# Optimization experiments

Measured on AMD Instinct MI355X. Metric: run time of the kernel, lower is better.

The kernel has to match this reference:

```python
import jax, jax.numpy as jnp
import numpy as np

B_SZ, SEQ, H, P = 4, 8192, 512, 256


def _s5(x, lam_re, lam_im, log_dt, b_re, b_im, c_re, c_im, d):
    """Single-direction S5 diagonal SSM. x: [B,L,H] -> y: [B,L,H]."""
    lam = lam_re + 1j * lam_im                      # [P] complex diagonal A
    dt = jnp.exp(log_dt)                            # [P] ZOH timestep
    a_bar = jnp.exp(lam * dt)                       # [P] discretized A
    b_bar = ((a_bar - 1.0) / lam)[:, None] * (b_re + 1j * b_im)  # [P,H]
    bu = jnp.einsum('blh,ph->blp', x.astype(b_bar.dtype), b_bar)  # [B,L,P]
    a_el = jnp.broadcast_to(a_bar, bu.shape)        # time-invariant A per step

    def comb(e1, e2):  # associative combine for linear recurrence
        a1, s1 = e1
        a2, s2 = e2
        return (a1 * a2, a2 * s1 + s2)

    _, states = jax.lax.associative_scan(comb, (a_el, bu), axis=1)  # [B,L,P]
    c = c_re + 1j * c_im                            # [H,P]
    return jnp.einsum('blp,hp->blh', states, c).real + x * d


def setup_inputs() -> dict:
    key = jax.random.key(0)
    ks = jax.random.split(key, 10)
    return {
        'x': jax.random.normal(ks[0], (B_SZ, SEQ, H), dtype=jnp.float32),
        'Lambda_re': -0.1 - 0.5 * jax.random.uniform(ks[1], (2, P), dtype=jnp.float32),
        'Lambda_im': jnp.pi * jax.random.normal(ks[2], (2, P), dtype=jnp.float32),
        'log_dt': jnp.log(0.001) + (jnp.log(0.1) - jnp.log(0.001)) * jax.random.uniform(ks[3], (2, P), dtype=jnp.float32),
        'B_re': jax.random.normal(ks[4], (2, P, H), dtype=jnp.float32) / np.sqrt(H),
        'B_im': jax.random.normal(ks[5], (2, P, H), dtype=jnp.float32) / np.sqrt(H),
        'C_re': jax.random.normal(ks[6], (2, H, P), dtype=jnp.float32) / np.sqrt(P),
        'C_im': jax.random.normal(ks[7], (2, H, P), dtype=jnp.float32) / np.sqrt(P),
        'D': jax.random.normal(ks[8], (2, H), dtype=jnp.float32),
    }


def reference(x, Lambda_re, Lambda_im, log_dt, B_re, B_im, C_re, C_im, D):
    # fwd(x) + flip(bwd(flip(x)))
    y_f = _s5(x, Lambda_re[0], Lambda_im[0], log_dt[0], B_re[0], B_im[0], C_re[0], C_im[0], D[0])
    x_r = x[:, ::-1]
    y_b = _s5(x_r, Lambda_re[1], Lambda_im[1], log_dt[1], B_re[1], B_im[1], C_re[1], C_im[1], D[1])[:, ::-1]
    return y_f + y_b
```

## Files before the change

kernel.cpp:

```cpp
#include <hip/hip_runtime.h>
#include <math.h>

typedef unsigned short ushort_t;
typedef __bf16 bf16x8 __attribute__((ext_vector_type(8)));
typedef ushort_t ushort8v __attribute__((ext_vector_type(8)));
typedef float f32x4 __attribute__((ext_vector_type(4)));

#define B_SZ   4
#define SEQ    8192
#define M_ROWS (B_SZ * SEQ)
#define CH     128
#define NC     (SEQ / CH)

__device__ __forceinline__ ushort_t f2bf(float f) {
    unsigned u = __float_as_uint(f);
    u = u + 0x7fffu + ((u >> 16) & 1u);
    return (ushort_t)(u >> 16);
}
__device__ __forceinline__ float bf2f(ushort_t b) {
    return __uint_as_float(((unsigned)b) << 16);
}

__device__ __forceinline__ void load16_lds(const void* g, void* l) {
    __builtin_amdgcn_global_load_lds(
        (const __attribute__((address_space(1))) unsigned int*)g,
        (__attribute__((address_space(3))) unsigned int*)l, 16, 0, 0);
}

__global__ void prep_kernel(const float* __restrict__ Lre,
                            const float* __restrict__ Lim,
                            const float* __restrict__ ldt,
                            const float* __restrict__ Bre,
                            const float* __restrict__ Bim,
                            const float* __restrict__ Cre,
                            const float* __restrict__ Cim,
                            float* __restrict__ abar,
                            float* __restrict__ apow,
                            ushort_t* __restrict__ Bmat,
                            ushort_t* __restrict__ Cmat) {
    int idx = blockIdx.x * 256 + threadIdx.x;
    int h = idx & 511;
    int p = (idx >> 9) & 255;
    int d = idx >> 17;
    int ip = d * 256 + p;
    float lr = Lre[ip], li = Lim[ip];
    float dt = expf(ldt[ip]);
    float e   = expf(lr * dt);
    float ang = li * dt;
    float ar = e * cosf(ang), ai = e * sinf(ang);
    float nr = ar - 1.0f, ni = ai;
    float den = lr * lr + li * li;
    float cr = (nr * lr + ni * li) / den;
    float ci = (ni * lr - nr * li) / den;
    float br = Bre[idx], bi = Bim[idx];
    Bmat[(d * 512 + 2 * p) * 512 + h]     = f2bf(cr * br - ci * bi);
    Bmat[(d * 512 + 2 * p + 1) * 512 + h] = f2bf(cr * bi + ci * br);
    if (h == 0) {
        int o = d * 512 + 2 * p;
        abar[o] = ar;  abar[o + 1] = ai;
        float eC = expf(lr * dt * (float)CH);
        float aC = ang * (float)CH;
        apow[o] = eC * cosf(aC);  apow[o + 1] = eC * sinf(aC);
    }
    int p2 = idx & 255;
    int h2 = (idx >> 8) & 511;
    int d2 = idx >> 17;
    Cmat[h2 * 1024 + d2 * 512 + 2 * p2]     = f2bf(Cre[idx]);
    Cmat[h2 * 1024 + d2 * 512 + 2 * p2 + 1] = f2bf(-Cim[idx]);
}

__global__ void conv_x_kernel(const float* __restrict__ x,
                              ushort_t* __restrict__ X16) {
    int i = blockIdx.x * 256 + threadIdx.x;
    float4 v = ((const float4*)x)[i];
    ushort_t o[4] = {f2bf(v.x), f2bf(v.y), f2bf(v.z), f2bf(v.w)};
    *(uint2*)&X16[(size_t)i * 4] = *(const uint2*)o;
}

template<int EPI, int KD_, int NT>
__global__ __launch_bounds__(256)
void gemm_mfma(const ushort_t* __restrict__ A, const ushort_t* __restrict__ Bm,
               ushort_t* __restrict__ Cb, float* __restrict__ Cf,
               const float* __restrict__ X, const float* __restrict__ Dv) {
    __shared__ ushort_t As[128 * 32];
    __shared__ ushort_t Bs[128 * 32];
    const int tid  = threadIdx.x;
    const int lane = tid & 63;
    const int wv   = tid >> 6;
    const int wrow = wv >> 1, wcol = wv & 1;
    const int l15  = lane & 15, lq = lane >> 4;

    const int lin = blockIdx.x;
    const int xcd = lin & 7;
    const int j   = lin >> 3;
    const int mt  = xcd * 32 + j / NT;
    const int nt  = j % NT;
    const int m0 = mt * 128;
    const int n0 = nt * 128;
    const int CN = NT * 128;

    f32x4 acc[4][4];
#pragma unroll
    for (int i = 0; i < 4; ++i)
#pragma unroll
        for (int jj = 0; jj < 4; ++jj)
            acc[i][jj] = (f32x4){0.f, 0.f, 0.f, 0.f};

    const int grow_l = lane >> 2;
    const int gk8    = (lane & 3) * 8;

    const ushort_t* aF = As + (wrow * 64 + l15) * 32 + lq * 8;
    const ushort_t* bF = Bs + (wcol * 64 + l15) * 32 + lq * 8;

    for (int kt = 0; kt < KD_; kt += 32) {
        __syncthreads();
#pragma unroll
        for (int j2 = 0; j2 < 2; ++j2) {
            const int r0 = j2 * 64 + wv * 16;
            load16_lds(&A[(size_t)(m0 + r0 + grow_l) * KD_ + kt + gk8],
                       (void*)&As[r0 * 32]);
            load16_lds(&Bm[(size_t)(n0 + r0 + grow_l) * KD_ + kt + gk8],
                       (void*)&Bs[r0 * 32]);
        }
        __syncthreads();

        bf16x8 af[4], bfr[4];
#pragma unroll
        for (int mi = 0; mi < 4; ++mi) {
            union { ushort8v u; bf16x8 b; } cv;
            cv.u = *(const ushort8v*)(aF + mi * 512);
            af[mi] = cv.b;
        }
#pragma unroll
        for (int ni = 0; ni < 4; ++ni) {
            union { ushort8v u; bf16x8 b; } cv;
            cv.u = *(const ushort8v*)(bF + ni * 512);
            bfr[ni] = cv.b;
        }
#pragma unroll
        for (int mi = 0; mi < 4; ++mi)
#pragma unroll
            for (int ni = 0; ni < 4; ++ni)
                acc[mi][ni] = __builtin_amdgcn_mfma_f32_16x16x32_bf16(
                    af[mi], bfr[ni], acc[mi][ni], 0, 0, 0);
    }

#pragma unroll
    for (int mi = 0; mi < 4; ++mi) {
#pragma unroll
        for (int ni = 0; ni < 4; ++ni) {
            const int col = n0 + wcol * 64 + ni * 16 + l15;
            float dsum = 0.f;
            if (EPI == 1) dsum = Dv[col] + Dv[512 + col];
#pragma unroll
            for (int r = 0; r < 4; ++r) {
                const int row = m0 + wrow * 64 + mi * 16 + lq * 4 + r;
                if (EPI == 0) {
                    Cb[(size_t)row * CN + col] = f2bf(acc[mi][ni][r]);
                } else {
                    const size_t idx = (size_t)row * 512 + col;
                    Cf[idx] = acc[mi][ni][r] + X[idx] * dsum;
                }
            }
        }
    }
}

__global__ __launch_bounds__(512)
void scan_carry(const ushort_t* __restrict__ S, const float* __restrict__ abar,
                float* __restrict__ carry) {
    int b = blockIdx.x, c = blockIdx.y, t = threadIdx.x;
    int dir = t >> 8, p = t & 255;
    float ar = abar[dir * 512 + 2 * p], ai = abar[dir * 512 + 2 * p + 1];
    float sr = 0.f, si = 0.f;
    const ushort_t* base = S + ((size_t)b * SEQ + (size_t)c * CH) * 1024
                             + dir * 512 + 2 * p;
    for (int ii = 0; ii < CH; ++ii) {
        int i = dir ? (CH - 1 - ii) : ii;
        unsigned u = *(const unsigned*)(base + (size_t)i * 1024);
        float re = bf2f((ushort_t)(u & 0xffffu));
        float im = bf2f((ushort_t)(u >> 16));
        float nr = fmaf(ar, sr, fmaf(-ai, si, re));
        float ni = fmaf(ar, si, fmaf(ai, sr, im));
        sr = nr; si = ni;
    }
    int o = (b * NC + c) * 1024 + dir * 512 + 2 * p;
    carry[o] = sr; carry[o + 1] = si;
}

__global__ __launch_bounds__(512)
void scan_comb(const float* __restrict__ carry, float* __restrict__ init,
               const float* __restrict__ apow) {
    int b = blockIdx.x, t = threadIdx.x;
    int dir = t >> 8, p = t & 255;
    float pr = apow[dir * 512 + 2 * p], pi = apow[dir * 512 + 2 * p + 1];
    float sr = 0.f, si = 0.f;
    for (int cc = 0; cc < NC; ++cc) {
        int c = dir ? (NC - 1 - cc) : cc;
        int o = (b * NC + c) * 1024 + dir * 512 + 2 * p;
        init[o] = sr; init[o + 1] = si;
        float cr = carry[o], ci = carry[o + 1];
        float nr = fmaf(pr, sr, fmaf(-pi, si, cr));
        float ni = fmaf(pr, si, fmaf(pi, sr, ci));
        sr = nr; si = ni;
    }
}

__global__ __launch_bounds__(512)
void scan_final(ushort_t* __restrict__ S, const float* __restrict__ abar,
                const float* __restrict__ init) {
    int b = blockIdx.x, c = blockIdx.y, t = threadIdx.x;
    int dir = t >> 8, p = t & 255;
    float ar = abar[dir * 512 + 2 * p], ai = abar[dir * 512 + 2 * p + 1];
    int o = (b * NC + c) * 1024 + dir * 512 + 2 * p;
    float sr = init[o], si = init[o + 1];
    ushort_t* base = S + ((size_t)b * SEQ + (size_t)c * CH) * 1024
                       + dir * 512 + 2 * p;
    for (int ii = 0; ii < CH; ++ii) {
        int i = dir ? (CH - 1 - ii) : ii;
        unsigned* addr = (unsigned*)(base + (size_t)i * 1024);
        unsigned u = *addr;
        float re = bf2f((ushort_t)(u & 0xffffu));
        float im = bf2f((ushort_t)(u >> 16));
        float nr = fmaf(ar, sr, fmaf(-ai, si, re));
        float ni = fmaf(ar, si, fmaf(ai, sr, im));
        sr = nr; si = ni;
        *addr = ((unsigned)f2bf(si) << 16) | (unsigned)f2bf(sr);
    }
}

extern "C" void kernel_launch(void* const* d_in, const int* in_sizes, int n_in,
                              void* d_out, int out_size, void* d_ws, size_t ws_size,
                              hipStream_t stream) {
    const float* x   = (const float*)d_in[0];
    const float* Lre = (const float*)d_in[1];
    const float* Lim = (const float*)d_in[2];
    const float* ldt = (const float*)d_in[3];
    const float* Bre = (const float*)d_in[4];
    const float* Bim = (const float*)d_in[5];
    const float* Cre = (const float*)d_in[6];
    const float* Cim = (const float*)d_in[7];
    const float* Dv  = (const float*)d_in[8];
    float* y = (float*)d_out;
    char* ws = (char*)d_ws;

    ushort_t* SB16 = (ushort_t*)(ws);
    ushort_t* X16  = (ushort_t*)(ws + 67108864);
    ushort_t* Bm16 = (ushort_t*)(ws + 100663296);
    ushort_t* Cm16 = (ushort_t*)(ws + 101711872);
    float* abar  = (float*)(ws + 102760448);
    float* apow  = (float*)(ws + 102764544);
    float* carry = (float*)(ws + 67108864);
    float* initb = (float*)(ws + 68157440);

    prep_kernel<<<1024, 256, 0, stream>>>(Lre, Lim, ldt, Bre, Bim, Cre, Cim,
                                          abar, apow, Bm16, Cm16);
    conv_x_kernel<<<16384, 256, 0, stream>>>(x, X16);

    gemm_mfma<0, 512, 8><<<2048, 256, 0, stream>>>(X16, Bm16, SB16, nullptr,
                                                   nullptr, nullptr);

    dim3 gs(B_SZ, NC);
    scan_carry<<<gs, 512, 0, stream>>>(SB16, abar, carry);
    scan_comb<<<B_SZ, 512, 0, stream>>>(carry, initb, apow);
    scan_final<<<gs, 512, 0, stream>>>(SB16, abar, initb);

    gemm_mfma<1, 1024, 4><<<1024, 256, 0, stream>>>(SB16, Cm16, nullptr, y,
                                                    x, Dv);
}
```

Before: 286.9 us.

## Fuse chunk-local scan into first GEMM epilogue and apply carries via power correction

The first GEMM now reads fp32 x directly and converts it to bf16 while staging into LDS, which removes the separate conversion pass. Its epilogue writes the output tile to LDS and runs the within-chunk complex recurrence there: four segment scans are combined through a precomputed a^32 power, then the chunk carry is emitted and locally scanned states are stored. The full-sequence re-scan is replaced by a parallel correction kernel that adds a^(l+1)·init (or the reverse power for the backward direction) from a precomputed power table. This trades two serial global scan passes over a large bf16 buffer for one elementwise pass, at the cost of more LDS use and a serial tail in the GEMM blocks.

```diff
diff --git a/kernel.cpp b/kernel.cpp
--- a/kernel.cpp
+++ b/kernel.cpp
@@ -36,6 +36,7 @@
                             const float* __restrict__ Cim,
                             float* __restrict__ abar,
                             float* __restrict__ apow,
+                            float* __restrict__ a32t,
                             ushort_t* __restrict__ Bmat,
                             ushort_t* __restrict__ Cmat) {
     int idx = blockIdx.x * 256 + threadIdx.x;
@@ -58,9 +59,12 @@
     if (h == 0) {
         int o = d * 512 + 2 * p;
         abar[o] = ar;  abar[o + 1] = ai;
-        float eC = expf(lr * dt * (float)CH);
-        float aC = ang * (float)CH;
+        float eC = expf(lr * dt * 128.f);
+        float aC = ang * 128.f;
         apow[o] = eC * cosf(aC);  apow[o + 1] = eC * sinf(aC);
+        float e32 = expf(lr * dt * 32.f);
+        float a32 = ang * 32.f;
+        a32t[o] = e32 * cosf(a32);  a32t[o + 1] = e32 * sinf(a32);
     }
     int p2 = idx & 255;
     int h2 = (idx >> 8) & 511;
@@ -69,21 +73,34 @@
     Cmat[h2 * 1024 + d2 * 512 + 2 * p2 + 1] = f2bf(-Cim[idx]);
 }
 
-__global__ void conv_x_kernel(const float* __restrict__ x,
-                              ushort_t* __restrict__ X16) {
-    int i = blockIdx.x * 256 + threadIdx.x;
-    float4 v = ((const float4*)x)[i];
-    ushort_t o[4] = {f2bf(v.x), f2bf(v.y), f2bf(v.z), f2bf(v.w)};
-    *(uint2*)&X16[(size_t)i * 4] = *(const uint2*)o;
-}
-
-template<int EPI, int KD_, int NT>
+__global__ void pw_kernel(const float* __restrict__ Lre,
+                          const float* __restrict__ Lim,
+                          const float* __restrict__ ldt,
+                          float* __restrict__ pw) {
+    int l  = blockIdx.x;
+    int pg = threadIdx.x;
+    int d = pg >> 8, p = pg & 255;
+    int ip = d * 256 + p;
+    float lr = Lre[ip], li = Lim[ip];
+    float dt = expf(ldt[ip]);
+    float ex = (d == 0) ? (float)(l + 1) : (float)(128 - l);
+    float mag = expf(lr * dt * ex);
+    float ang = li * dt * ex;
+    pw[(l * 512 + pg) * 2]     = mag * cosf(ang);
+    pw[(l * 512 + pg) * 2 + 1] = mag * sinf(ang);
+}
+
 __global__ __launch_bounds__(256)
-void gemm_mfma(const ushort_t* __restrict__ A, const ushort_t* __restrict__ Bm,
-               ushort_t* __restrict__ Cb, float* __restrict__ Cf,
-               const float* __restrict__ X, const float* __restrict__ Dv) {
-    __shared__ ushort_t As[128 * 32];
-    __shared__ ushort_t Bs[128 * 32];
+void gemm1_scan(const float* __restrict__ Xf, const ushort_t* __restrict__ Bm,
+                ushort_t* __restrict__ SB, const float* __restrict__ abar,
+                const float* __restrict__ a32t, float* __restrict__ carry) {
+    __shared__ __align__(16) char ldsraw[36864];
+    ushort_t* As      = (ushort_t*)ldsraw;
+    ushort_t* Bs      = (ushort_t*)(ldsraw + 8192);
+    ushort_t* scanbuf = (ushort_t*)ldsraw;
+    float*    segE    = (float*)(ldsraw + 32768);
+    float*    cin     = (float*)(ldsraw + 34816);
+
     const int tid  = threadIdx.x;
     const int lane = tid & 63;
     const int wv   = tid >> 6;
@@ -93,11 +110,10 @@
     const int lin = blockIdx.x;
     const int xcd = lin & 7;
     const int j   = lin >> 3;
-    const int mt  = xcd * 32 + j / NT;
-    const int nt  = j % NT;
+    const int mt  = xcd * 32 + (j >> 3);
+    const int nt  = j & 7;
     const int m0 = mt * 128;
     const int n0 = nt * 128;
-    const int CN = NT * 128;
 
     f32x4 acc[4][4];
 #pragma unroll
@@ -109,19 +125,32 @@
     const int grow_l = lane >> 2;
     const int gk8    = (lane & 3) * 8;
 
+    const int arow = tid >> 1;
+    const int akh  = (tid & 1) << 4;
+    const float* Ap = &Xf[(size_t)(m0 + arow) * 512 + akh];
+
     const ushort_t* aF = As + (wrow * 64 + l15) * 32 + lq * 8;
     const ushort_t* bF = Bs + (wcol * 64 + l15) * 32 + lq * 8;
 
-    for (int kt = 0; kt < KD_; kt += 32) {
+    for (int kt = 0; kt < 512; kt += 32) {
+        float4 a0 = *(const float4*)(Ap + kt);
+        float4 a1 = *(const float4*)(Ap + kt + 4);
+        float4 a2 = *(const float4*)(Ap + kt + 8);
+        float4 a3 = *(const float4*)(Ap + kt + 12);
         __syncthreads();
 #pragma unroll
         for (int j2 = 0; j2 < 2; ++j2) {
             const int r0 = j2 * 64 + wv * 16;
-            load16_lds(&A[(size_t)(m0 + r0 + grow_l) * KD_ + kt + gk8],
-                       (void*)&As[r0 * 32]);
-            load16_lds(&Bm[(size_t)(n0 + r0 + grow_l) * KD_ + kt + gk8],
+            load16_lds(&Bm[(size_t)(n0 + r0 + grow_l) * 512 + kt + gk8],
                        (void*)&Bs[r0 * 32]);
         }
+        ushort8v w0, w1;
+        w0[0] = f2bf(a0.x); w0[1] = f2bf(a0.y); w0[2] = f2bf(a0.z); w0[3] = f2bf(a0.w);
+        w0[4] = f2bf(a1.x); w0[5] = f2bf(a1.y); w0[6] = f2bf(a1.z); w0[7] = f2bf(a1.w);
+        w1[0] = f2bf(a2.x); w1[1] = f2bf(a2.y); w1[2] = f2bf(a2.z); w1[3] = f2bf(a2.w);
+        w1[4] = f2bf(a3.x); w1[5] = f2bf(a3.y); w1[6] = f2bf(a3.z); w1[7] = f2bf(a3.w);
+        *(ushort8v*)&As[arow * 32 + akh]     = w0;
+        *(ushort8v*)&As[arow * 32 + akh + 8] = w1;
         __syncthreads();
 
         bf16x8 af[4], bfr[4];
@@ -145,47 +174,73 @@
                     af[mi], bfr[ni], acc[mi][ni], 0, 0, 0);
     }
 
-#pragma unroll
-    for (int mi = 0; mi < 4; ++mi) {
+    __syncthreads();
+#pragma unroll
+    for (int mi = 0; mi < 4; ++mi)
 #pragma unroll
         for (int ni = 0; ni < 4; ++ni) {
-            const int col = n0 + wcol * 64 + ni * 16 + l15;
-            float dsum = 0.f;
-            if (EPI == 1) dsum = Dv[col] + Dv[512 + col];
+            const int col = wcol * 64 + ni * 16 + l15;
 #pragma unroll
             for (int r = 0; r < 4; ++r) {
-                const int row = m0 + wrow * 64 + mi * 16 + lq * 4 + r;
-                if (EPI == 0) {
-                    Cb[(size_t)row * CN + col] = f2bf(acc[mi][ni][r]);
-                } else {
-                    const size_t idx = (size_t)row * 512 + col;
-                    Cf[idx] = acc[mi][ni][r] + X[idx] * dsum;
-                }
+                const int row = wrow * 64 + mi * 16 + lq * 4 + r;
+                scanbuf[row * 128 + col] = f2bf(acc[mi][ni][r]);
             }
         }
-    }
-}
-
-__global__ __launch_bounds__(512)
-void scan_carry(const ushort_t* __restrict__ S, const float* __restrict__ abar,
-                float* __restrict__ carry) {
-    int b = blockIdx.x, c = blockIdx.y, t = threadIdx.x;
-    int dir = t >> 8, p = t & 255;
-    float ar = abar[dir * 512 + 2 * p], ai = abar[dir * 512 + 2 * p + 1];
+    __syncthreads();
+
+    const int ch = tid & 63;
+    const int sg = tid >> 6;
+    const int pg = (n0 >> 1) + ch;
+    const bool bwd = (pg >= 256);
+    const float ar = abar[2 * pg], ai = abar[2 * pg + 1];
+
     float sr = 0.f, si = 0.f;
-    const ushort_t* base = S + ((size_t)b * SEQ + (size_t)c * CH) * 1024
-                             + dir * 512 + 2 * p;
-    for (int ii = 0; ii < CH; ++ii) {
-        int i = dir ? (CH - 1 - ii) : ii;
-        unsigned u = *(const unsigned*)(base + (size_t)i * 1024);
+    for (int i = 0; i < 32; ++i) {
+        int l = sg * 32 + i;
+        int row = bwd ? (127 - l) : l;
+        unsigned u = *(const unsigned*)&scanbuf[row * 128 + 2 * ch];
         float re = bf2f((ushort_t)(u & 0xffffu));
         float im = bf2f((ushort_t)(u >> 16));
         float nr = fmaf(ar, sr, fmaf(-ai, si, re));
-        float ni = fmaf(ar, si, fmaf(ai, sr, im));
-        sr = nr; si = ni;
-    }
-    int o = (b * NC + c) * 1024 + dir * 512 + 2 * p;
-    carry[o] = sr; carry[o + 1] = si;
+        float ni2 = fmaf(ar, si, fmaf(ai, sr, im));
+        sr = nr; si = ni2;
+    }
+    segE[(ch * 4 + sg) * 2]     = sr;
+    segE[(ch * 4 + sg) * 2 + 1] = si;
+    __syncthreads();
+
+    if (sg == 0) {
+        const float pr = a32t[2 * pg], pi = a32t[2 * pg + 1];
+        float er = 0.f, ei = 0.f;
+        for (int s2 = 0; s2 < 4; ++s2) {
+            cin[(ch * 4 + s2) * 2]     = er;
+            cin[(ch * 4 + s2) * 2 + 1] = ei;
+            float cr = segE[(ch * 4 + s2) * 2];
+            float ci = segE[(ch * 4 + s2) * 2 + 1];
+            float nr = fmaf(pr, er, fmaf(-pi, ei, cr));
+            float ni2 = fmaf(pr, ei, fmaf(pi, er, ci));
+            er = nr; ei = ni2;
+        }
+        carry[mt * 1024 + 2 * pg]     = er;
+        carry[mt * 1024 + 2 * pg + 1] = ei;
+    }
+    __syncthreads();
+
+    sr = cin[(ch * 4 + sg) * 2];
+    si = cin[(ch * 4 + sg) * 2 + 1];
+    ushort_t* outp = SB + (size_t)m0 * 1024 + n0 + 2 * ch;
+    for (int i = 0; i < 32; ++i) {
+        int l = sg * 32 + i;
+        int row = bwd ? (127 - l) : l;
+        unsigned u = *(const unsigned*)&scanbuf[row * 128 + 2 * ch];
+        float re = bf2f((ushort_t)(u & 0xffffu));
+        float im = bf2f((ushort_t)(u >> 16));
+        float nr = fmaf(ar, sr, fmaf(-ai, si, re));
+        float ni2 = fmaf(ar, si, fmaf(ai, sr, im));
+        sr = nr; si = ni2;
+        *(unsigned*)(outp + (size_t)row * 1024) =
+            ((unsigned)f2bf(si) << 16) | (unsigned)f2bf(sr);
+    }
 }
 
 __global__ __launch_bounds__(512)
@@ -206,27 +261,118 @@
     }
 }
 
-__global__ __launch_bounds__(512)
-void scan_final(ushort_t* __restrict__ S, const float* __restrict__ abar,
-                const float* __restrict__ init) {
-    int b = blockIdx.x, c = blockIdx.y, t = threadIdx.x;
-    int dir = t >> 8, p = t & 255;
-    float ar = abar[dir * 512 + 2 * p], ai = abar[dir * 512 + 2 * p + 1];
-    int o = (b * NC + c) * 1024 + dir * 512 + 2 * p;
-    float sr = init[o], si = init[o + 1];
-    ushort_t* base = S + ((size_t)b * SEQ + (size_t)c * CH) * 1024
-                       + dir * 512 + 2 * p;
-    for (int ii = 0; ii < CH; ++ii) {
-        int i = dir ? (CH - 1 - ii) : ii;
-        unsigned* addr = (unsigned*)(base + (size_t)i * 1024);
-        unsigned u = *addr;
-        float re = bf2f((ushort_t)(u & 0xffffu));
-        float im = bf2f((ushort_t)(u >> 16));
-        float nr = fmaf(ar, sr, fmaf(-ai, si, re));
-        float ni = fmaf(ar, si, fmaf(ai, sr, im));
-        sr = nr; si = ni;
-        *addr = ((unsigned)f2bf(si) << 16) | (unsigned)f2bf(sr);
-    }
+__global__ __launch_bounds__(256)
+void correct_kernel(ushort_t* __restrict__ SB, const float* __restrict__ pw,
+                    const float* __restrict__ initb) {
+    unsigned tid = blockIdx.x * 256 + threadIdx.x;
+    int m  = tid >> 7;
+    int k8 = (tid & 127) * 8;
+    int lrow  = m & 127;
+    int chunk = m >> 7;
+    ushort_t* sp = SB + (size_t)m * 1024 + k8;
+    uint4 sv = *(const uint4*)sp;
+    unsigned uu[4] = {sv.x, sv.y, sv.z, sv.w};
+    const float* pwp = pw + ((size_t)lrow * 512 + (k8 >> 1)) * 2;
+    const float* inp = initb + (size_t)chunk * 1024 + k8;
+    float4 pw0 = *(const float4*)pwp;
+    float4 pw1 = *(const float4*)(pwp + 4);
+    float4 in0 = *(const float4*)inp;
+    float4 in1 = *(const float4*)(inp + 4);
+    float pr[4] = {pw0.x, pw0.z, pw1.x, pw1.z};
+    float pi[4] = {pw0.y, pw0.w, pw1.y, pw1.w};
+    float ir[4] = {in0.x, in0.z, in1.x, in1.z};
+    float ii[4] = {in0.y, in0.w, in1.y, in1.w};
+#pragma unroll
+    for (int q = 0; q < 4; ++q) {
+        float sr = bf2f((ushort_t)(uu[q] & 0xffffu));
+        float si = bf2f((ushort_t)(uu[q] >> 16));
+        sr = fmaf(pr[q], ir[q], fmaf(-pi[q], ii[q], sr));
+        si = fmaf(pr[q], ii[q], fmaf(pi[q], ir[q], si));
+        uu[q] = ((unsigned)f2bf(si) << 16) | (unsigned)f2bf(sr);
+    }
+    uint4 ov = {uu[0], uu[1], uu[2], uu[3]};
+    *(uint4*)sp = ov;
+}
+
+__global__ __launch_bounds__(256)
+void gemm2_mfma(const ushort_t* __restrict__ A, const ushort_t* __restrict__ Bm,
+                float* __restrict__ Cf, const float* __restrict__ X,
+                const float* __restrict__ Dv) {
+    __shared__ ushort_t As[128 * 32];
+    __shared__ ushort_t Bs[128 * 32];
+    const int tid  = threadIdx.x;
+    const int lane = tid & 63;
+    const int wv   = tid >> 6;
+    const int wrow = wv >> 1, wcol = wv & 1;
+    const int l15  = lane & 15, lq = lane >> 4;
+
+    const int lin = blockIdx.x;
+    const int xcd = lin & 7;
+    const int j   = lin >> 3;
+    const int mt  = xcd * 32 + (j >> 2);
+    const int nt  = j & 3;
+    const int m0 = mt * 128;
+    const int n0 = nt * 128;
+
+    f32x4 acc[4][4];
+#pragma unroll
+    for (int i = 0; i < 4; ++i)
+#pragma unroll
+        for (int jj = 0; jj < 4; ++jj)
+            acc[i][jj] = (f32x4){0.f, 0.f, 0.f, 0.f};
+
+    const int grow_l = lane >> 2;
+    const int gk8    = (lane & 3) * 8;
+
+    const ushort_t* aF = As + (wrow * 64 + l15) * 32 + lq * 8;
+    const ushort_t* bF = Bs + (wcol * 64 + l15) * 32 + lq * 8;
+
+    for (int kt = 0; kt < 1024; kt += 32) {
+        __syncthreads();
+#pragma unroll
+        for (int j2 = 0; j2 < 2; ++j2) {
+            const int r0 = j2 * 64 + wv * 16;
+            load16_lds(&A[(size_t)(m0 + r0 + grow_l) * 1024 + kt + gk8],
+                       (void*)&As[r0 * 32]);
+            load16_lds(&Bm[(size_t)(n0 + r0 + grow_l) * 1024 + kt + gk8],
+                       (void*)&Bs[r0 * 32]);
+        }
+        __syncthreads();
+
+        bf16x8 af[4], bfr[4];
+#pragma unroll
+        for (int mi = 0; mi < 4; ++mi) {
+            union { ushort8v u; bf16x8 b; } cv;
+            cv.u = *(const ushort8v*)(aF + mi * 512);
+            af[mi] = cv.b;
+        }
+#pragma unroll
+        for (int ni = 0; ni < 4; ++ni) {
+            union { ushort8v u; bf16x8 b; } cv;
+            cv.u = *(const ushort8v*)(bF + ni * 512);
+            bfr[ni] = cv.b;
+        }
+#pragma unroll
+        for (int mi = 0; mi < 4; ++mi)
+#pragma unroll
+            for (int ni = 0; ni < 4; ++ni)
+                acc[mi][ni] = __builtin_amdgcn_mfma_f32_16x16x32_bf16(
+                    af[mi], bfr[ni], acc[mi][ni], 0, 0, 0);
+    }
+
+#pragma unroll
+    for (int mi = 0; mi < 4; ++mi)
+#pragma unroll
+        for (int ni = 0; ni < 4; ++ni) {
+            const int col = n0 + wcol * 64 + ni * 16 + l15;
+            const float dsum = Dv[col] + Dv[512 + col];
+#pragma unroll
+            for (int r = 0; r < 4; ++r) {
+                const int row = m0 + wrow * 64 + mi * 16 + lq * 4 + r;
+                const size_t idx = (size_t)row * 512 + col;
+                Cf[idx] = acc[mi][ni][r] + X[idx] * dsum;
+            }
+        }
 }
 
 extern "C" void kernel_launch(void* const* d_in, const int* in_sizes, int n_in,
@@ -244,27 +390,22 @@
     float* y = (float*)d_out;
     char* ws = (char*)d_ws;
 
-    ushort_t* SB16 = (ushort_t*)(ws);
-    ushort_t* X16  = (ushort_t*)(ws + 67108864);
-    ushort_t* Bm16 = (ushort_t*)(ws + 100663296);
-    ushort_t* Cm16 = (ushort_t*)(ws + 101711872);
-    float* abar  = (float*)(ws + 102760448);
-    float* apow  = (float*)(ws + 102764544);
-    float* carry = (float*)(ws + 67108864);
-    float* initb = (float*)(ws + 68157440);
+    ushort_t* SB   = (ushort_t*)(ws);
+    ushort_t* Bm16 = (ushort_t*)(ws + 67108864);
+    ushort_t* Cm16 = (ushort_t*)(ws + 68157440);
+    float* abar  = (float*)(ws + 69206016);
+    float* apow  = (float*)(ws + 69210112);
+    float* a32t  = (float*)(ws + 69214208);
+    float* pw    = (float*)(ws + 69218304);
+    float* carry = (float*)(ws + 69742592);
+    float* initb = (float*)(ws + 70791168);
 
     prep_kernel<<<1024, 256, 0, stream>>>(Lre, Lim, ldt, Bre, Bim, Cre, Cim,
-                                          abar, apow, Bm16, Cm16);
-    conv_x_kernel<<<16384, 256, 0, stream>>>(x, X16);
-
-    gemm_mfma<0, 512, 8><<<2048, 256, 0, stream>>>(X16, Bm16, SB16, nullptr,
-                                                   nullptr, nullptr);
-
-    dim3 gs(B_SZ, NC);
-    scan_carry<<<gs, 512, 0, stream>>>(SB16, abar, carry);
+                                          abar, apow, a32t, Bm16, Cm16);
+    pw_kernel<<<128, 512, 0, stream>>>(Lre, Lim, ldt, pw);
+
+    gemm1_scan<<<2048, 256, 0, stream>>>(x, Bm16, SB, abar, a32t, carry);
     scan_comb<<<B_SZ, 512, 0, stream>>>(carry, initb, apow);
-    scan_final<<<gs, 512, 0, stream>>>(SB16, abar, initb);
-
-    gemm_mfma<1, 1024, 4><<<1024, 256, 0, stream>>>(SB16, Cm16, nullptr, y,
-                                                    x, Dv);
-}
+    correct_kernel<<<16384, 256, 0, stream>>>(SB, pw, initb);
+    gemm2_mfma<<<1024, 256, 0, stream>>>(SB, Cm16, y, x, Dv);
+}
```

Result: slower. 315.6 us (+10.0%).
